# Optimization experiments

Measured on AMD Instinct MI355X. Metric: run time of the kernel, lower is better.

The kernel has to match this reference:

```python
import jax, jax.numpy as jnp
import numpy as np

N = 32768   # nodes
E = 524288  # edges (avg degree 16)
F = 32      # num_features
H = 512     # hidden_channels
C = 10      # num_classes
G = 64      # graphs in batch


def setup_inputs() -> dict:
    key = jax.random.key(0)
    ks = jax.random.split(key, 16)
    s = 0.05  # weight init scale
    f32 = jnp.float32
    return {
        "x": jax.random.normal(ks[0], (N, F), f32),
        "edge_index": jax.random.randint(ks[1], (2, E), 0, N),
        "batch_index": jnp.sort(jax.random.randint(ks[2], (N,), 0, G)),
        # initial_conv: F -> H  (PyG GraphConv: lin_root on x, lin_rel on aggregated neighbors)
        "w_root0": jax.random.normal(ks[3], (F, H), f32) * s,
        "w_rel0": jax.random.normal(ks[4], (F, H), f32) * s,
        "b0": jnp.zeros((H,), f32),
        # conv1..conv4 stacked: H -> H
        "w_root": jax.random.normal(ks[5], (4, H, H), f32) * s,
        "w_rel": jax.random.normal(ks[6], (4, H, H), f32) * s,
        "b": jnp.zeros((4, H), f32),
        # MLP tail
        "lin1_w": jax.random.normal(ks[7], (2 * H, H), f32) * s,
        "lin1_b": jnp.zeros((H,), f32),
        "lin2_w": jax.random.normal(ks[8], (H, H), f32) * s,
        "lin2_b": jnp.zeros((H,), f32),
        "lin3_w": jax.random.normal(ks[9], (H, C), f32) * s,
        "lin3_b": jnp.zeros((C,), f32),
    }


def _graph_conv(h, src, dst, w_root, w_rel, bias):
    # out_i = h_i @ W_root + (sum_{j->i} h_j) @ W_rel + b   (PyG GraphConv, aggr='add')
    agg = jax.ops.segment_sum(h[src], dst, num_segments=N)
    return h @ w_root + agg @ w_rel + bias


def reference(x, edge_index, batch_index,
              w_root0, w_rel0, b0, w_root, w_rel, b,
              lin1_w, lin1_b, lin2_w, lin2_b, lin3_w, lin3_b):
    src, dst = edge_index[0], edge_index[1]
    h = jnp.tanh(_graph_conv(x, src, dst, w_root0, w_rel0, b0))
    for i in range(4):  # fixed small layer loop
        h = jnp.tanh(_graph_conv(h, src, dst, w_root[i], w_rel[i], b[i]))
    # global max + mean pool over graphs
    gmax = jax.ops.segment_max(h, batch_index, num_segments=G)
    gsum = jax.ops.segment_sum(h, batch_index, num_segments=G)
    cnt = jax.ops.segment_sum(jnp.ones((N,), h.dtype), batch_index, num_segments=G)
    gmean = gsum / jnp.maximum(cnt, 1.0)[:, None]
    g = jnp.concatenate([gmax, gmean], axis=1)  # [G, 2H]
    # dropout is identity at inference (training=False)
    g = jnp.tanh(g @ lin1_w + lin1_b)
    g = jnp.tanh(g @ lin2_w + lin2_b)
    logits = g @ lin3_w + lin3_b
    return jax.nn.log_softmax(logits, axis=1)
```

## Files before the change

### kernel.cpp

```cpp
#include <hip/hip_runtime.h>
#include <hip/hip_bf16.h>
#include <math.h>

#define NN 32768
#define EE 524288
#define FF 32
#define HH 512
#define GG 64
#define CC 10

typedef __attribute__((ext_vector_type(8))) short short8;
typedef __attribute__((ext_vector_type(4))) float floatx4;
typedef __attribute__((ext_vector_type(4))) unsigned int uintx4;

__device__ __forceinline__ float bf16_to_f32(unsigned short u) {
    union { unsigned int u; float f; } v;
    v.u = ((unsigned int)u) << 16;
    return v.f;
}
__device__ __forceinline__ unsigned short f32_to_bf16(float f) {
    union { float f; unsigned int u; } v;
    v.f = f;
    unsigned int u = v.u;
    u += 0x7FFFu + ((u >> 16) & 1u);
    return (unsigned short)(u >> 16);
}
__device__ __forceinline__ float fast_tanh(float x) {
    float e = __expf(2.0f * x);
    return 1.0f - 2.0f * __builtin_amdgcn_rcpf(e + 1.0f);
}

__global__ __launch_bounds__(256) void prep_all_kernel(const float* __restrict__ wr0, const float* __restrict__ wl0,
                                unsigned short* __restrict__ WT0,
                                const float* __restrict__ wroot, const float* __restrict__ wrel,
                                unsigned short* __restrict__ WTs,
                                const float* __restrict__ x, unsigned short* __restrict__ X0,
                                int* __restrict__ counts) {
    const int b = blockIdx.x;
    const int tid = threadIdx.x;
    if (b < 520) {
        __shared__ unsigned short tile[64][65];
        const int ty = tid >> 6, tx = tid & 63;
        if (b < 8) {
            const int n0 = b * 64;
#pragma unroll
            for (int q = 0; q < 16; ++q) {
                const int k = ty * 16 + q;
                const float v = (k < 32) ? wr0[k * 512 + n0 + tx]
                                         : wl0[(k - 32) * 512 + n0 + tx];
                tile[k][tx] = f32_to_bf16(v);
            }
            __syncthreads();
#pragma unroll
            for (int q = 0; q < 16; ++q) {
                const int n = n0 + ty * 16 + q;
                WT0[n * 64 + tx] = tile[tx][ty * 16 + q];
            }
        } else {
            const int bb = b - 8;
            const int l = bb >> 7;
            const int r = bb & 127;
            const int k0 = (r >> 3) * 64;
            const int n0 = (r & 7) * 64;
            const float* Wl = (k0 < 512) ? wroot + (size_t)l * 262144
                                         : wrel + (size_t)l * 262144;
            const int kb = (k0 < 512) ? k0 : k0 - 512;
#pragma unroll
            for (int q = 0; q < 16; ++q) {
                const int kk = ty * 16 + q;
                tile[kk][tx] = f32_to_bf16(Wl[(size_t)(kb + kk) * 512 + n0 + tx]);
            }
            __syncthreads();
#pragma unroll
            for (int q = 0; q < 16; ++q) {
                const int n = n0 + ty * 16 + q;
                WTs[(size_t)l * 524288 + (size_t)n * 1024 + k0 + tx] = tile[tx][ty * 16 + q];
            }
        }
    } else if (b < 4616) {
        const int t = (b - 520) * 256 + tid;
        const int i = t >> 5, c = t & 31;
        X0[(size_t)i * 64 + c] = f32_to_bf16(x[t]);
    } else {
        const int t4 = (b - 4616) * 256 + tid;
        if (t4 < 8320) {
            int4 z; z.x = 0; z.y = 0; z.z = 0; z.w = 0;
            ((int4*)counts)[t4] = z;
        }
    }
}

__global__ void hist_kernel(const int* __restrict__ dst, int* __restrict__ counts) {
    int e = blockIdx.x * blockDim.x + threadIdx.x;
    if (e < EE) atomicAdd(&counts[dst[e]], 1);
}

__global__ __launch_bounds__(256) void deg_hist_kernel(const int* __restrict__ counts,
                                                       int* __restrict__ degHist) {
    __shared__ int lh[256];
    lh[threadIdx.x] = 0;
    __syncthreads();
    int i = blockIdx.x * 256 + threadIdx.x;
    int d = counts[i]; if (d > 255) d = 255;
    atomicAdd(&lh[255 - d], 1);
    __syncthreads();
    int v = lh[threadIdx.x];
    if (v) atomicAdd(&degHist[threadIdx.x], v);
}

__global__ __launch_bounds__(256) void deg_scatter_kernel(const int* __restrict__ counts,
                                                          const int* __restrict__ degHist,
                                                          int* __restrict__ degBump,
                                                          int* __restrict__ perm,
                                                          int* __restrict__ pDeg,
                                                          int* __restrict__ iperm) {
    __shared__ int lh[256];
    __shared__ int sh[256];
    __shared__ int base[256];
    const int t = threadIdx.x;
    lh[t] = 0;
    const int own = degHist[t];
    sh[t] = own;
    __syncthreads();
    for (int off = 1; off < 256; off <<= 1) {
        int v = (t >= off) ? sh[t - off] : 0;
        __syncthreads();
        sh[t] += v;
        __syncthreads();
    }
    const int excl = sh[t] - own;
    int i = blockIdx.x * 256 + t;
    int dtrue = counts[i];
    int d = dtrue > 255 ? 255 : dtrue;
    int bin = 255 - d;
    int lr = atomicAdd(&lh[bin], 1);
    __syncthreads();
    int c = lh[t];
    if (c) base[t] = excl + atomicAdd(&degBump[t], c);
    __syncthreads();
    int p = base[bin] + lr;
    perm[p] = i;
    pDeg[p] = dtrue;
    iperm[i] = p;
}
__global__ __launch_bounds__(1024) void scan_kernel(const int* __restrict__ pDeg,
                                                    int* __restrict__ pRowStart,
                                                    int* __restrict__ pCursor) {
    __shared__ int part[1024];
    const int t = threadIdx.x;
    const int base = t * 32;
    int local[32];
    const int4* cp = (const int4*)(pDeg + base);
    int s = 0;
#pragma unroll
    for (int ii = 0; ii < 8; ++ii) {
        int4 v = cp[ii];
        local[ii * 4 + 0] = v.x; local[ii * 4 + 1] = v.y;
        local[ii * 4 + 2] = v.z; local[ii * 4 + 3] = v.w;
        s += v.x + v.y + v.z + v.w;
    }
    part[t] = s;
    __syncthreads();
    for (int off = 1; off < 1024; off <<= 1) {
        int v = (t >= off) ? part[t - off] : 0;
        __syncthreads();
        part[t] += v;
        __syncthreads();
    }
    int run = part[t] - s;
#pragma unroll
    for (int i = 0; i < 32; ++i) {
        pRowStart[base + i] = run;
        pCursor[base + i] = run;
        run += local[i];
    }
    if (t == 1023) pRowStart[NN] = run;
}

__global__ void scatter_kernel(const int* __restrict__ src, const int* __restrict__ dst,
                               const int* __restrict__ iperm,
                               int* __restrict__ pCursor, int* __restrict__ pssrc) {
    int e = blockIdx.x * blockDim.x + threadIdx.x;
    if (e < EE) {
        int p = iperm[dst[e]];
        int q = atomicAdd(&pCursor[p], 1);
        pssrc[q] = src[e];
    }
}

__device__ __forceinline__ void acc8(float* a, uint4 d) {
    a[0] += bf16_to_f32((unsigned short)(d.x & 0xFFFFu));
    a[1] += bf16_to_f32((unsigned short)(d.x >> 16));
    a[2] += bf16_to_f32((unsigned short)(d.y & 0xFFFFu));
    a[3] += bf16_to_f32((unsigned short)(d.y >> 16));
    a[4] += bf16_to_f32((unsigned short)(d.z & 0xFFFFu));
    a[5] += bf16_to_f32((unsigned short)(d.z >> 16));
    a[6] += bf16_to_f32((unsigned short)(d.w & 0xFFFFu));
    a[7] += bf16_to_f32((unsigned short)(d.w >> 16));
}
__device__ __forceinline__ void acc8v(float* a, uintx4 d) {
    a[0] += bf16_to_f32((unsigned short)(d[0] & 0xFFFFu));
    a[1] += bf16_to_f32((unsigned short)(d[0] >> 16));
    a[2] += bf16_to_f32((unsigned short)(d[1] & 0xFFFFu));
    a[3] += bf16_to_f32((unsigned short)(d[1] >> 16));
    a[4] += bf16_to_f32((unsigned short)(d[2] & 0xFFFFu));
    a[5] += bf16_to_f32((unsigned short)(d[2] >> 16));
    a[6] += bf16_to_f32((unsigned short)(d[3] & 0xFFFFu));
    a[7] += bf16_to_f32((unsigned short)(d[3] >> 16));
}

__global__ __launch_bounds__(256) void agg_kernel(const unsigned short* __restrict__ Xh,
                                                  unsigned short* __restrict__ Xagg,
                                                  const int* __restrict__ pRowStart,
                                                  const int* __restrict__ pssrc,
                                                  const int* __restrict__ perm) {
    const int p = blockIdx.x * 64 + (threadIdx.x >> 2);
    const int lc = threadIdx.x & 3;
    const int node = perm[p];
    const int s = pRowStart[p];
    const int e = pRowStart[p + 1];
    float a[8] = {0.f, 0.f, 0.f, 0.f, 0.f, 0.f, 0.f, 0.f};
    const unsigned short* base = Xh + lc * 8;
    int i = s;
    for (; i + 4 <= e; i += 4) {
        int j0 = pssrc[i], j1 = pssrc[i + 1], j2 = pssrc[i + 2], j3 = pssrc[i + 3];
        uint4 d0 = *(const uint4*)(base + (size_t)j0 * 64);
        uint4 d1 = *(const uint4*)(base + (size_t)j1 * 64);
        uint4 d2 = *(const uint4*)(base + (size_t)j2 * 64);
        uint4 d3 = *(const uint4*)(base + (size_t)j3 * 64);
        acc8(a, d0); acc8(a, d1); acc8(a, d2); acc8(a, d3);
    }
    for (; i < e; ++i) {
        int j = pssrc[i];
        uint4 d = *(const uint4*)(base + (size_t)j * 64);
        acc8(a, d);
    }
    unsigned short* out = Xagg + (size_t)node * 64 + lc * 8;
#pragma unroll
    for (int c = 0; c < 8; ++c) out[c] = f32_to_bf16(a[c]);
}

#define GLOAD(dreg, voff) \
    asm volatile("buffer_load_dwordx4 %0, %1, %2, 0 offen" \
                 : "=v"(dreg) : "v"(voff), "s"(srsrc))

__global__ __launch_bounds__(256, 3) void agg_slice_kernel(const unsigned short* __restrict__ Xh,
                                                           unsigned short* __restrict__ Xagg,
                                                           const int* __restrict__ pRowStart,
                                                           const int* __restrict__ pssrc,
                                                           const int* __restrict__ perm) {
    const int slice = blockIdx.x & 7;
    const int pair = blockIdx.x >> 3;
    const int wv = threadIdx.x >> 6;
    const int lane = threadIdx.x & 63;
    const int ln = lane >> 3;
    const int lc = lane & 7;
    const int colOff = slice * 64 + lc * 8;
    const unsigned short* base = Xh + colOff;
    uintx4 srsrc;
    {
        union { const unsigned short* p; unsigned int u[2]; } ba;
        ba.p = Xh + slice * 64;
        srsrc[0] = ba.u[0];
        srsrc[1] = ba.u[1] & 0xFFFFu;
        srsrc[2] = 0xFFFFFFFFu;
        srsrc[3] = 0x00020000u;
    }
    const unsigned int lcoff = (unsigned int)(lc << 4);
#pragma unroll
    for (int half = 0; half < 2; ++half) {
        const int nb = half ? (1023 - pair) : pair;
        const int p = nb * 32 + wv * 8 + ln;
        const int node = perm[p];
        const int s = pRowStart[p];
        const int e = pRowStart[p + 1];
        float a[8] = {0.f, 0.f, 0.f, 0.f, 0.f, 0.f, 0.f, 0.f};
        int i = s;
        for (; i + 16 <= e; i += 16) {
            unsigned int vo[16];
#pragma unroll
            for (int u = 0; u < 16; ++u)
                vo[u] = (((unsigned int)pssrc[i + u]) << 11) | lcoff;
            uintx4 d0, d1, d2, d3, d4, d5, d6, d7, d8, d9, d10, d11, d12, d13, d14, d15;
            __builtin_amdgcn_sched_barrier(0);
            GLOAD(d0, vo[0]);   GLOAD(d1, vo[1]);   GLOAD(d2, vo[2]);   GLOAD(d3, vo[3]);
            GLOAD(d4, vo[4]);   GLOAD(d5, vo[5]);   GLOAD(d6, vo[6]);   GLOAD(d7, vo[7]);
            GLOAD(d8, vo[8]);   GLOAD(d9, vo[9]);   GLOAD(d10, vo[10]); GLOAD(d11, vo[11]);
            GLOAD(d12, vo[12]); GLOAD(d13, vo[13]); GLOAD(d14, vo[14]); GLOAD(d15, vo[15]);
            asm volatile("s_waitcnt vmcnt(8)" ::: "memory");
            __builtin_amdgcn_sched_barrier(0);
            acc8v(a, d0); acc8v(a, d1); acc8v(a, d2); acc8v(a, d3);
            acc8v(a, d4); acc8v(a, d5); acc8v(a, d6); acc8v(a, d7);
            asm volatile("s_waitcnt vmcnt(0)" ::: "memory");
            __builtin_amdgcn_sched_barrier(0);
            acc8v(a, d8);  acc8v(a, d9);  acc8v(a, d10); acc8v(a, d11);
            acc8v(a, d12); acc8v(a, d13); acc8v(a, d14); acc8v(a, d15);
        }
        if (e - i >= 8) {
            unsigned int vo[8];
#pragma unroll
            for (int u = 0; u < 8; ++u)
                vo[u] = (((unsigned int)pssrc[i + u]) << 11) | lcoff;
            uintx4 d0, d1, d2, d3, d4, d5, d6, d7;
            __builtin_amdgcn_sched_barrier(0);
            GLOAD(d0, vo[0]); GLOAD(d1, vo[1]); GLOAD(d2, vo[2]); GLOAD(d3, vo[3]);
            GLOAD(d4, vo[4]); GLOAD(d5, vo[5]); GLOAD(d6, vo[6]); GLOAD(d7, vo[7]);
            asm volatile("s_waitcnt vmcnt(4)" ::: "memory");
            __builtin_amdgcn_sched_barrier(0);
            acc8v(a, d0); acc8v(a, d1); acc8v(a, d2); acc8v(a, d3);
            asm volatile("s_waitcnt vmcnt(0)" ::: "memory");
            __builtin_amdgcn_sched_barrier(0);
            acc8v(a, d4); acc8v(a, d5); acc8v(a, d6); acc8v(a, d7);
            i += 8;
        }
        for (; i + 4 <= e; i += 4) {
            int j0 = pssrc[i], j1 = pssrc[i + 1], j2 = pssrc[i + 2], j3 = pssrc[i + 3];
            uint4 e0 = *(const uint4*)(base + (size_t)j0 * 1024);
            uint4 e1 = *(const uint4*)(base + (size_t)j1 * 1024);
            uint4 e2 = *(const uint4*)(base + (size_t)j2 * 1024);
            uint4 e3 = *(const uint4*)(base + (size_t)j3 * 1024);
            acc8(a, e0); acc8(a, e1); acc8(a, e2); acc8(a, e3);
        }
        for (; i < e; ++i) {
            int j = pssrc[i];
            uint4 d = *(const uint4*)(base + (size_t)j * 1024);
            acc8(a, d);
        }
        unsigned short* out = Xagg + (size_t)node * 1024 + colOff;
#pragma unroll
        for (int c = 0; c < 8; ++c) out[c] = f32_to_bf16(a[c]);
    }
}

__global__ __launch_bounds__(256, 4) void gemm_bias_tanh(const unsigned short* __restrict__ Xin,
                                                         int ldin, int K,
                                                         const unsigned short* __restrict__ WT,
                                                         const float* __restrict__ bias,
                                                         unsigned short* __restrict__ Xout,
                                                         int ldout) {
    __shared__ __align__(16) unsigned short As[128 * 64];
    __shared__ __align__(16) unsigned short Bs[128 * 64];
    const int tid = threadIdx.x;
    const int lane = tid & 63;
    const int wave = tid >> 6;
    const int wm = wave >> 1, wn = wave & 1;
    const int bm = blockIdx.x, bn = blockIdx.y;

    floatx4 acc[4][4] = {};

    const int lrow = lane >> 3;
    const int schunk = (lane & 7) ^ (lrow & 7);
    const unsigned short* Abase = Xin + (size_t)(bm * 128) * ldin;
    const unsigned short* Bbase = WT + (size_t)(bn * 128) * K;
    const int m = lane & 15;
    const int quad = lane >> 4;

    for (int k0 = 0; k0 < K; k0 += 64) {
        __syncthreads();
#pragma unroll
        for (int q = 0; q < 4; ++q) {
            const int rr = q * 32 + wave * 8;
            const int row = rr + lrow;
            const unsigned short* sa = Abase + (size_t)row * ldin + (k0 + schunk * 8);
            const unsigned short* sb = Bbase + (size_t)row * K + (k0 + schunk * 8);
            __builtin_amdgcn_global_load_lds(
                (const __attribute__((address_space(1))) void*)sa,
                (__attribute__((address_space(3))) void*)(&As[rr * 64]), 16, 0, 0);
            __builtin_amdgcn_global_load_lds(
                (const __attribute__((address_space(1))) void*)sb,
                (__attribute__((address_space(3))) void*)(&Bs[rr * 64]), 16, 0, 0);
        }
        __syncthreads();
#pragma unroll
        for (int half = 0; half < 2; ++half) {
            short8 af[4], bfr[4];
#pragma unroll
            for (int t = 0; t < 4; ++t) {
                const int row = wm * 64 + t * 16 + m;
                const int chunk = (half * 4 + quad) ^ (row & 7);
                af[t] = *(const short8*)&As[row * 64 + chunk * 8];
            }
#pragma unroll
            for (int t = 0; t < 4; ++t) {
                const int row = wn * 64 + t * 16 + m;
                const int chunk = (half * 4 + quad) ^ (row & 7);
                bfr[t] = *(const short8*)&Bs[row * 64 + chunk * 8];
            }
#pragma unroll
            for (int mt = 0; mt < 4; ++mt)
#pragma unroll
                for (int nt = 0; nt < 4; ++nt)
                    acc[mt][nt] = __builtin_amdgcn_mfma_f32_16x16x32_bf16(af[mt], bfr[nt],
                                                                          acc[mt][nt], 0, 0, 0);
        }
    }

    const int row0 = bm * 128 + wm * 64;
    const int col0 = bn * 128 + wn * 64;
#pragma unroll
    for (int mt = 0; mt < 4; ++mt) {
#pragma unroll
        for (int nt = 0; nt < 4; ++nt) {
            const int col = col0 + nt * 16 + m;
            const float bv = bias[col];
#pragma unroll
            for (int r = 0; r < 4; ++r) {
                const int row = row0 + mt * 16 + quad * 4 + r;
                float v = fast_tanh(acc[mt][nt][r] + bv);
                Xout[(size_t)row * ldout + col] = f32_to_bf16(v);
            }
        }
    }
}

__device__ __forceinline__ void stage_half(const unsigned short* __restrict__ gsrc0,
                                           int ldg, unsigned short* ldsHalf,
                                           int w, int lane) {
#pragma unroll
    for (int q = 0; q < 2; ++q) {
        const int rb = q * 64 + w * 8;
        const unsigned short* src = gsrc0 + (size_t)(rb + (lane >> 3)) * ldg
                                    + ((lane & 7) ^ (lane >> 3)) * 8;
        __builtin_amdgcn_global_load_lds(
            (const __attribute__((address_space(1))) void*)src,
            (__attribute__((address_space(3))) void*)(ldsHalf + rb * 64), 16, 0, 0);
    }
}
__device__ __forceinline__ void stage_q(const unsigned short* __restrict__ gsrc0,
                                        int ldg, unsigned short* ldsQ,
                                        int w, int lane) {
    const unsigned short* src = gsrc0 + (size_t)(w * 8 + (lane >> 3)) * ldg
                                + ((lane & 7) ^ (lane >> 3)) * 8;
    __builtin_amdgcn_global_load_lds(
        (const __attribute__((address_space(1))) void*)src,
        (__attribute__((address_space(3))) void*)(ldsQ + (w * 8) * 64), 16, 0, 0);
}

__global__ __launch_bounds__(512, 2) void gemm256_bias_tanh(
    const unsigned short* __restrict__ Xin, int ldin, int K,
    const unsigned short* __restrict__ WT, const float* __restrict__ bias,
    unsigned short* __restrict__ Xout, int ldout) {
    __shared__ __align__(16) unsigned short As[2][256 * 64];
    __shared__ __align__(16) unsigned short Bs[2][256 * 64];
    const int tid = threadIdx.x;
    const int lane = tid & 63;
    const int w = tid >> 6;
    const int wm = w >> 2, wn = w & 3;
    const int m = lane & 15, quad = lane >> 4;
    const int id = (int)blockIdx.x;
    const int bm = (id & 7) * 16 + (id >> 4);
    const int bn = (id >> 3) & 1;
    const int NT = K >> 6;

    const unsigned short* Abase = Xin + (size_t)(bm * 256) * ldin;
    const unsigned short* Bbase = WT + (size_t)(bn * 256) * K;

    floatx4 acc[8][4] = {};

#define STG_AH(buf, h, kt_) stage_half(Abase + (size_t)((h) * 128) * ldin + (kt_) * 64, ldin, \
                                       &As[buf][(h) * 128 * 64], w, lane)
#define STG_BH(buf, h, kt_) stage_half(Bbase + (size_t)((h) * 128) * K + (kt_) * 64, K, \
                                       &Bs[buf][(h) * 128 * 64], w, lane)
#define STG_AQ(buf, qr, kt_) stage_q(Abase + (size_t)((qr) * 64) * ldin + (kt_) * 64, ldin, \
                                     &As[buf][(qr) * 64 * 64], w, lane)

    STG_BH(0, 0, 0); STG_BH(0, 1, 0); STG_AH(0, 0, 0); STG_AH(0, 1, 0);
    STG_BH(1, 0, 1); STG_BH(1, 1, 1); STG_AH(1, 0, 1); STG_AH(1, 1, 1);
    asm volatile("s_waitcnt vmcnt(8)" ::: "memory");
    __builtin_amdgcn_s_barrier();

    for (int kt = 0; kt < NT; ++kt) {
        const int cur = kt & 1;
        const unsigned short* Ac = &As[cur][0];
        const unsigned short* Bc = &Bs[cur][0];
        const bool pf = (kt + 2 < NT);
        short8 afr[8], bfr[8];

#pragma unroll
        for (int nf = 0; nf < 4; ++nf)
#pragma unroll
            for (int ks = 0; ks < 2; ++ks) {
                const int col = wn * 64 + nf * 16 + m;
                const int chunk = (ks * 4 + quad) ^ (col & 7);
                bfr[nf * 2 + ks] = *(const short8*)&Bc[col * 64 + chunk * 8];
            }
#pragma unroll
        for (int t = 0; t < 4; ++t)
#pragma unroll
            for (int ks = 0; ks < 2; ++ks) {
                const int row = wm * 128 + t * 16 + m;
                const int chunk = (ks * 4 + quad) ^ (row & 7);
                afr[t * 2 + ks] = *(const short8*)&Ac[row * 64 + chunk * 8];
            }
        __builtin_amdgcn_s_barrier();
        __builtin_amdgcn_s_setprio(1);
#pragma unroll
        for (int t = 0; t < 4; ++t)
#pragma unroll
            for (int u = 0; u < 2; ++u)
#pragma unroll
                for (int ks = 0; ks < 2; ++ks)
                    acc[t][u] = __builtin_amdgcn_mfma_f32_16x16x32_bf16(
                        afr[t * 2 + ks], bfr[u * 2 + ks], acc[t][u], 0, 0, 0);
        __builtin_amdgcn_s_setprio(0);
        __builtin_amdgcn_s_barrier();

        if (pf) { STG_AQ(cur, 0, kt + 2); STG_AQ(cur, 2, kt + 2); }
        __builtin_amdgcn_s_barrier();
        __builtin_amdgcn_s_setprio(1);
#pragma unroll
        for (int t = 0; t < 4; ++t)
#pragma unroll
            for (int u = 2; u < 4; ++u)
#pragma unroll
                for (int ks = 0; ks < 2; ++ks)
                    acc[t][u] = __builtin_amdgcn_mfma_f32_16x16x32_bf16(
                        afr[t * 2 + ks], bfr[u * 2 + ks], acc[t][u], 0, 0, 0);
        __builtin_amdgcn_s_setprio(0);
        __builtin_amdgcn_s_barrier();

#pragma unroll
        for (int t = 0; t < 4; ++t)
#pragma unroll
            for (int ks = 0; ks < 2; ++ks) {
                const int row = wm * 128 + (4 + t) * 16 + m;
                const int chunk = (ks * 4 + quad) ^ (row & 7);
                afr[t * 2 + ks] = *(const short8*)&Ac[row * 64 + chunk * 8];
            }
        __builtin_amdgcn_sched_barrier(0);
        if (pf) STG_BH(cur, 0, kt + 2);
        __builtin_amdgcn_s_barrier();
        __builtin_amdgcn_s_setprio(1);
#pragma unroll
        for (int t = 0; t < 4; ++t)
#pragma unroll
            for (int u = 0; u < 2; ++u)
#pragma unroll
                for (int ks = 0; ks < 2; ++ks)
                    acc[4 + t][u] = __builtin_amdgcn_mfma_f32_16x16x32_bf16(
                        afr[t * 2 + ks], bfr[u * 2 + ks], acc[4 + t][u], 0, 0, 0);
        __builtin_amdgcn_s_setprio(0);
        __builtin_amdgcn_s_barrier();

        if (pf) {
            STG_BH(cur, 1, kt + 2);
            STG_AQ(cur, 1, kt + 2); STG_AQ(cur, 3, kt + 2);
        }
        __builtin_amdgcn_s_barrier();
        __builtin_amdgcn_s_setprio(1);
#pragma unroll
        for (int t = 0; t < 4; ++t)
#pragma unroll
            for (int u = 2; u < 4; ++u)
#pragma unroll
                for (int ks = 0; ks < 2; ++ks)
                    acc[4 + t][u] = __builtin_amdgcn_mfma_f32_16x16x32_bf16(
                        afr[t * 2 + ks], bfr[u * 2 + ks], acc[4 + t][u], 0, 0, 0);
        __builtin_amdgcn_s_setprio(0);
        if (kt <= NT - 3) {
            asm volatile("s_waitcnt vmcnt(8)" ::: "memory");
        } else {
            asm volatile("s_waitcnt vmcnt(0)" ::: "memory");
        }
        __builtin_amdgcn_s_barrier();
    }
#undef STG_AH
#undef STG_BH
#undef STG_AQ

    const int row0 = bm * 256 + wm * 128;
    const int col0 = bn * 256 + wn * 64;
#pragma unroll
    for (int mf = 0; mf < 8; ++mf) {
#pragma unroll
        for (int nf = 0; nf < 4; ++nf) {
            const int col = col0 + nf * 16 + m;
            const float bv = bias[col];
#pragma unroll
            for (int r = 0; r < 4; ++r) {
                const int row = row0 + mf * 16 + quad * 4 + r;
                float v = fast_tanh(acc[mf][nf][r] + bv);
                Xout[(size_t)row * ldout + col] = f32_to_bf16(v);
            }
        }
    }
}

__global__ __launch_bounds__(256) void pool_partial(const unsigned short* __restrict__ h,
                                                    const int* __restrict__ batch,
                                                    float* __restrict__ part) {
    const int gi = blockIdx.x, rs = blockIdx.y, t = threadIdx.x;
    int lo = 0, hi = NN;
    while (lo < hi) { int mid = (lo + hi) >> 1; if (batch[mid] < gi) lo = mid + 1; else hi = mid; }
    const int start = lo;
    hi = NN;
    while (lo < hi) { int mid = (lo + hi) >> 1; if (batch[mid] < gi + 1) lo = mid + 1; else hi = mid; }
    const int end = lo;
    const int len = end - start;
    const int q = (len + 7) >> 3;
    int r0 = start + rs * q;
    int r1 = r0 + q; if (r1 > end) r1 = end; if (r0 > end) r0 = end;
    float mx0 = -INFINITY, mx1 = -INFINITY, s0 = 0.f, s1 = 0.f;
    int i = r0;
    for (; i + 2 <= r1; i += 2) {
        unsigned int d0 = *(const unsigned int*)(h + (size_t)i * 1024 + t * 2);
        unsigned int d1 = *(const unsigned int*)(h + (size_t)(i + 1) * 1024 + t * 2);
        float v0 = bf16_to_f32((unsigned short)(d0 & 0xFFFFu));
        float v1 = bf16_to_f32((unsigned short)(d0 >> 16));
        float w0 = bf16_to_f32((unsigned short)(d1 & 0xFFFFu));
        float w1 = bf16_to_f32((unsigned short)(d1 >> 16));
        mx0 = fmaxf(mx0, fmaxf(v0, w0)); mx1 = fmaxf(mx1, fmaxf(v1, w1));
        s0 += v0 + w0; s1 += v1 + w1;
    }
    for (; i < r1; ++i) {
        unsigned int d0 = *(const unsigned int*)(h + (size_t)i * 1024 + t * 2);
        float v0 = bf16_to_f32((unsigned short)(d0 & 0xFFFFu));
        float v1 = bf16_to_f32((unsigned short)(d0 >> 16));
        mx0 = fmaxf(mx0, v0); mx1 = fmaxf(mx1, v1);
        s0 += v0; s1 += v1;
    }
    float* p = part + ((size_t)gi * 8 + rs) * 1024;
    p[t * 2] = mx0; p[t * 2 + 1] = mx1;
    p[512 + t * 2] = s0; p[512 + t * 2 + 1] = s1;
}

__global__ __launch_bounds__(256) void pool_combine(const float* __restrict__ part,
                                                    const int* __restrict__ batch,
                                                    float* __restrict__ gT) {
    const int gi = blockIdx.x, t = threadIdx.x;
    int lo = 0, hi = NN;
    while (lo < hi) { int mid = (lo + hi) >> 1; if (batch[mid] < gi) lo = mid + 1; else hi = mid; }
    const int start = lo;
    hi = NN;
    while (lo < hi) { int mid = (lo + hi) >> 1; if (batch[mid] < gi + 1) lo = mid + 1; else hi = mid; }
    int cnt = lo - start; if (cnt < 1) cnt = 1;
    const float inv = 1.0f / (float)cnt;
    float mx0 = -INFINITY, mx1 = -INFINITY, s0 = 0.f, s1 = 0.f;
#pragma unroll
    for (int rs = 0; rs < 8; ++rs) {
        const float* p = part + ((size_t)gi * 8 + rs) * 1024;
        mx0 = fmaxf(mx0, p[t * 2]); mx1 = fmaxf(mx1, p[t * 2 + 1]);
        s0 += p[512 + t * 2]; s1 += p[512 + t * 2 + 1];
    }
    gT[(size_t)(2 * t) * 64 + gi]        = mx0;
    gT[(size_t)(2 * t + 1) * 64 + gi]    = mx1;
    gT[(size_t)(512 + 2 * t) * 64 + gi]  = s0 * inv;
    gT[(size_t)(512 + 2 * t + 1) * 64 + gi] = s1 * inv;
}

__global__ __launch_bounds__(256) void mlp_splitk(const float* __restrict__ ginT,
                                                  const float* __restrict__ W,
                                                  int Ndim,
                                                  float* __restrict__ partial) {
    __shared__ float gsT[64][68];
    __shared__ float Ws[64][68];
    const int t = threadIdx.x;
    const int wv = t >> 6, l = t & 63;
    const int nb = blockIdx.x, kb = blockIdx.y;
    const int n0 = nb * 64;
    const int gr = t >> 2;
    const int c4 = (t & 3) * 16;
    float acc[16] = {};
#pragma unroll
    for (int sub = 0; sub < 2; ++sub) {
        const int k0 = kb * 128 + sub * 64;
        __syncthreads();
        {
            const float4* gsrc = (const float4*)(ginT + (size_t)(k0 + gr) * 64 + c4);
            float4* gd = (float4*)&gsT[gr][c4];
            gd[0] = gsrc[0]; gd[1] = gsrc[1]; gd[2] = gsrc[2]; gd[3] = gsrc[3];
            const float4* wsrc = (const float4*)(W + (size_t)(k0 + gr) * Ndim + n0 + c4);
            float4* wd = (float4*)&Ws[gr][c4];
            wd[0] = wsrc[0]; wd[1] = wsrc[1]; wd[2] = wsrc[2]; wd[3] = wsrc[3];
        }
        __syncthreads();
#pragma unroll 4
        for (int kk = 0; kk < 64; ++kk) {
            const float wval = Ws[kk][l];
            const float4* gv = (const float4*)&gsT[kk][wv * 16];
            float4 g0 = gv[0], g1 = gv[1], g2 = gv[2], g3 = gv[3];
            acc[0]  = fmaf(g0.x, wval, acc[0]);  acc[1]  = fmaf(g0.y, wval, acc[1]);
            acc[2]  = fmaf(g0.z, wval, acc[2]);  acc[3]  = fmaf(g0.w, wval, acc[3]);
            acc[4]  = fmaf(g1.x, wval, acc[4]);  acc[5]  = fmaf(g1.y, wval, acc[5]);
            acc[6]  = fmaf(g1.z, wval, acc[6]);  acc[7]  = fmaf(g1.w, wval, acc[7]);
            acc[8]  = fmaf(g2.x, wval, acc[8]);  acc[9]  = fmaf(g2.y, wval, acc[9]);
            acc[10] = fmaf(g2.z, wval, acc[10]); acc[11] = fmaf(g2.w, wval, acc[11]);
            acc[12] = fmaf(g3.x, wval, acc[12]); acc[13] = fmaf(g3.y, wval, acc[13]);
            acc[14] = fmaf(g3.z, wval, acc[14]); acc[15] = fmaf(g3.w, wval, acc[15]);
        }
    }
    float* p = partial + ((size_t)kb * 64) * Ndim;
#pragma unroll
    for (int g = 0; g < 16; ++g)
        p[(size_t)(wv * 16 + g) * Ndim + n0 + l] = acc[g];
}

__global__ __launch_bounds__(256) void mlp_combine(const float* __restrict__ partial, int nparts,
                                                   const float* __restrict__ bias, int Ndim,
                                                   float* __restrict__ outN,
                                                   float* __restrict__ outT) {
    const int idx = blockIdx.x * 256 + threadIdx.x;
    if (idx >= 64 * Ndim) return;
    const int g = idx / Ndim, n = idx - g * Ndim;
    float s = bias[n];
    for (int kb = 0; kb < nparts; ++kb)
        s += partial[((size_t)kb * 64 + g) * Ndim + n];
    const float v = fast_tanh(s);
    if (outN) outN[(size_t)g * Ndim + n] = v;
    if (outT) outT[(size_t)n * 64 + g] = v;
}

__global__ __launch_bounds__(64) void head_kernel(const float* __restrict__ g2,
                                                  const float* __restrict__ W,
                                                  const float* __restrict__ b,
                                                  float* __restrict__ out) {
    const int gi = blockIdx.x, t = threadIdx.x;
    const float4* gp = (const float4*)(g2 + (size_t)gi * HH + t * 8);
    float4 ga = gp[0], gb = gp[1];
    float gv[8] = {ga.x, ga.y, ga.z, ga.w, gb.x, gb.y, gb.z, gb.w};
    float logits[CC];
#pragma unroll
    for (int c = 0; c < CC; ++c) {
        float p = 0.f;
#pragma unroll
        for (int j = 0; j < 8; ++j)
            p = fmaf(gv[j], W[(t * 8 + j) * CC + c], p);
#pragma unroll
        for (int off = 32; off > 0; off >>= 1)
            p += __shfl_xor(p, off, 64);
        logits[c] = p + b[c];
    }
    if (t == 0) {
        float mx = logits[0];
#pragma unroll
        for (int c = 1; c < CC; ++c) mx = fmaxf(mx, logits[c]);
        float s = 0.f;
#pragma unroll
        for (int c = 0; c < CC; ++c) s += expf(logits[c] - mx);
        float lse = mx + logf(s);
#pragma unroll
        for (int c = 0; c < CC; ++c) out[(size_t)gi * CC + c] = logits[c] - lse;
    }
}

extern "C" void kernel_launch(void* const* d_in, const int* in_sizes, int n_in,
                              void* d_out, int out_size, void* d_ws, size_t ws_size,
                              hipStream_t stream) {
    const float* x       = (const float*)d_in[0];
    const int*   ei      = (const int*)d_in[1];
    const int*   batch   = (const int*)d_in[2];
    const float* w_root0 = (const float*)d_in[3];
    const float* w_rel0  = (const float*)d_in[4];
    const float* b0      = (const float*)d_in[5];
    const float* w_root  = (const float*)d_in[6];
    const float* w_rel   = (const float*)d_in[7];
    const float* bvec    = (const float*)d_in[8];
    const float* lin1_w  = (const float*)d_in[9];
    const float* lin1_b  = (const float*)d_in[10];
    const float* lin2_w  = (const float*)d_in[11];
    const float* lin2_b  = (const float*)d_in[12];
    const float* lin3_w  = (const float*)d_in[13];
    const float* lin3_b  = (const float*)d_in[14];
    float* out = (float*)d_out;

    char* w = (char*)d_ws;
    size_t off = 0;
    auto alloc = [&](size_t bytes) -> char* {
        char* p = w + off;
        off += (bytes + 255) & ~(size_t)255;
        return p;
    };
    unsigned short* Xa  = (unsigned short*)alloc((size_t)NN * 1024 * 2);
    unsigned short* Xb  = (unsigned short*)alloc((size_t)NN * 1024 * 2);
    unsigned short* X0  = (unsigned short*)alloc((size_t)NN * 64 * 2);
    unsigned short* WT0 = (unsigned short*)alloc(512 * 64 * 2);
    unsigned short* WTs = (unsigned short*)alloc((size_t)4 * 512 * 1024 * 2);
    int* counts   = (int*)alloc((size_t)(NN + 512) * 4);
    int* degHist  = counts + NN;
    int* degBump  = counts + NN + 256;
    int* perm     = (int*)alloc((size_t)NN * 4);
    int* pDeg     = (int*)alloc((size_t)NN * 4);
    int* iperm    = (int*)alloc((size_t)NN * 4);
    int* pRowStart= (int*)alloc((size_t)(NN + 1) * 4);
    int* pCursor  = (int*)alloc((size_t)NN * 4);
    int* pssrc    = (int*)alloc((size_t)EE * 4);
    float* gbufT  = (float*)alloc((size_t)1024 * 64 * 4);
    float* g1T    = (float*)alloc((size_t)512 * 64 * 4);
    float* g2buf  = (float*)alloc((size_t)GG * 512 * 4);
    float* mlpPart = (float*)alloc((size_t)8 * 64 * 512 * 4);
    float* part   = (float*)X0;

    const int* esrc = ei;
    const int* edst = ei + EE;

    prep_all_kernel<<<4649, 256, 0, stream>>>(w_root0, w_rel0, WT0, w_root, w_rel, WTs, x, X0, counts);
    hist_kernel<<<2048, 256, 0, stream>>>(edst, counts);
    deg_hist_kernel<<<128, 256, 0, stream>>>(counts, degHist);
    deg_scatter_kernel<<<128, 256, 0, stream>>>(counts, degHist, degBump, perm, pDeg, iperm);
    scan_kernel<<<1, 1024, 0, stream>>>(pDeg, pRowStart, pCursor);
    scatter_kernel<<<2048, 256, 0, stream>>>(esrc, edst, iperm, pCursor, pssrc);

    agg_kernel<<<512, 256, 0, stream>>>(X0, X0 + 32, pRowStart, pssrc, perm);
    gemm_bias_tanh<<<dim3(256, 4), 256, 0, stream>>>(X0, 64, 64, WT0, b0, Xa, 1024);

    agg_slice_kernel<<<4096, 256, 0, stream>>>(Xa, Xa + 512, pRowStart, pssrc, perm);
    gemm256_bias_tanh<<<256, 512, 0, stream>>>(Xa, 1024, 1024, WTs + 0 * 524288, bvec + 0, Xb, 1024);
    agg_slice_kernel<<<4096, 256, 0, stream>>>(Xb, Xb + 512, pRowStart, pssrc, perm);
    gemm256_bias_tanh<<<256, 512, 0, stream>>>(Xb, 1024, 1024, WTs + 1 * 524288, bvec + 512, Xa, 1024);
    agg_slice_kernel<<<4096, 256, 0, stream>>>(Xa, Xa + 512, pRowStart, pssrc, perm);
    gemm256_bias_tanh<<<256, 512, 0, stream>>>(Xa, 1024, 1024, WTs + 2 * 524288, bvec + 1024, Xb, 1024);
    agg_slice_kernel<<<4096, 256, 0, stream>>>(Xb, Xb + 512, pRowStart, pssrc, perm);
    gemm256_bias_tanh<<<256, 512, 0, stream>>>(Xb, 1024, 1024, WTs + 3 * 524288, bvec + 1536, Xa, 1024);

    pool_partial<<<dim3(GG, 8), 256, 0, stream>>>(Xa, batch, part);
    pool_combine<<<GG, 256, 0, stream>>>(part, batch, gbufT);
    mlp_splitk<<<dim3(8, 8), 256, 0, stream>>>(gbufT, lin1_w, 512, mlpPart);
    mlp_combine<<<128, 256, 0, stream>>>(mlpPart, 8, lin1_b, 512, nullptr, g1T);
    mlp_splitk<<<dim3(8, 4), 256, 0, stream>>>(g1T, lin2_w, 512, mlpPart);
    mlp_combine<<<128, 256, 0, stream>>>(mlpPart, 4, lin2_b, 512, g2buf, nullptr);
    head_kernel<<<GG, 64, 0, stream>>>(g2buf, lin3_w, lin3_b, out);
}
```

Measured before the change: 578.8 us.

## Replace interleaved staged GEMM pipeline with simple one-ahead double buffering

The 256x256 bias+tanh GEMM kernel drops its split-phase schedule. That schedule staged A quarter-tiles and B halves two k-tiles ahead, spread across four MFMA sub-phases with s_setprio and explicit vmcnt waits. It now prefetches the whole next k-tile at the top of each iteration, runs all MFMAs in two blocks, and ends each iteration with one __syncthreads. This removes many barriers and priority toggles and simplifies the code. In exchange, prefetch distance drops from two tiles to one, and each iteration waits for all outstanding loads at the barrier, so global-to-LDS latency is less well hidden.

```diff
diff --git a/kernel.cpp b/kernel.cpp
--- a/kernel.cpp
+++ b/kernel.cpp
@@ -426,15 +426,6 @@
             (__attribute__((address_space(3))) void*)(ldsHalf + rb * 64), 16, 0, 0);
     }
 }
-__device__ __forceinline__ void stage_q(const unsigned short* __restrict__ gsrc0,
-                                        int ldg, unsigned short* ldsQ,
-                                        int w, int lane) {
-    const unsigned short* src = gsrc0 + (size_t)(w * 8 + (lane >> 3)) * ldg
-                                + ((lane & 7) ^ (lane >> 3)) * 8;
-    __builtin_amdgcn_global_load_lds(
-        (const __attribute__((address_space(1))) void*)src,
-        (__attribute__((address_space(3))) void*)(ldsQ + (w * 8) * 64), 16, 0, 0);
-}
 
 __global__ __launch_bounds__(512, 2) void gemm256_bias_tanh(
     const unsigned short* __restrict__ Xin, int ldin, int K,
@@ -457,25 +448,22 @@
 
     floatx4 acc[8][4] = {};
 
-#define STG_AH(buf, h, kt_) stage_half(Abase + (size_t)((h) * 128) * ldin + (kt_) * 64, ldin, \
-                                       &As[buf][(h) * 128 * 64], w, lane)
-#define STG_BH(buf, h, kt_) stage_half(Bbase + (size_t)((h) * 128) * K + (kt_) * 64, K, \
-                                       &Bs[buf][(h) * 128 * 64], w, lane)
-#define STG_AQ(buf, qr, kt_) stage_q(Abase + (size_t)((qr) * 64) * ldin + (kt_) * 64, ldin, \
-                                     &As[buf][(qr) * 64 * 64], w, lane)
-
-    STG_BH(0, 0, 0); STG_BH(0, 1, 0); STG_AH(0, 0, 0); STG_AH(0, 1, 0);
-    STG_BH(1, 0, 1); STG_BH(1, 1, 1); STG_AH(1, 0, 1); STG_AH(1, 1, 1);
-    asm volatile("s_waitcnt vmcnt(8)" ::: "memory");
-    __builtin_amdgcn_s_barrier();
+#define STG_T(buf, kt_) do { \
+        stage_half(Bbase + (kt_) * 64, K, &Bs[buf][0], w, lane); \
+        stage_half(Bbase + (size_t)128 * K + (kt_) * 64, K, &Bs[buf][128 * 64], w, lane); \
+        stage_half(Abase + (kt_) * 64, ldin, &As[buf][0], w, lane); \
+        stage_half(Abase + (size_t)128 * ldin + (kt_) * 64, ldin, &As[buf][128 * 64], w, lane); \
+    } while (0)
+
+    STG_T(0, 0);
+    __syncthreads();
 
     for (int kt = 0; kt < NT; ++kt) {
         const int cur = kt & 1;
+        if (kt + 1 < NT) STG_T(cur ^ 1, kt + 1);
         const unsigned short* Ac = &As[cur][0];
         const unsigned short* Bc = &Bs[cur][0];
-        const bool pf = (kt + 2 < NT);
-        short8 afr[8], bfr[8];
-
+        short8 bfr[8], afr[8];
 #pragma unroll
         for (int nf = 0; nf < 4; ++nf)
 #pragma unroll
@@ -492,33 +480,14 @@
                 const int chunk = (ks * 4 + quad) ^ (row & 7);
                 afr[t * 2 + ks] = *(const short8*)&Ac[row * 64 + chunk * 8];
             }
-        __builtin_amdgcn_s_barrier();
-        __builtin_amdgcn_s_setprio(1);
 #pragma unroll
         for (int t = 0; t < 4; ++t)
 #pragma unroll
-            for (int u = 0; u < 2; ++u)
+            for (int u = 0; u < 4; ++u)
 #pragma unroll
                 for (int ks = 0; ks < 2; ++ks)
                     acc[t][u] = __builtin_amdgcn_mfma_f32_16x16x32_bf16(
                         afr[t * 2 + ks], bfr[u * 2 + ks], acc[t][u], 0, 0, 0);
-        __builtin_amdgcn_s_setprio(0);
-        __builtin_amdgcn_s_barrier();
-
-        if (pf) { STG_AQ(cur, 0, kt + 2); STG_AQ(cur, 2, kt + 2); }
-        __builtin_amdgcn_s_barrier();
-        __builtin_amdgcn_s_setprio(1);
-#pragma unroll
-        for (int t = 0; t < 4; ++t)
-#pragma unroll
-            for (int u = 2; u < 4; ++u)
-#pragma unroll
-                for (int ks = 0; ks < 2; ++ks)
-                    acc[t][u] = __builtin_amdgcn_mfma_f32_16x16x32_bf16(
-                        afr[t * 2 + ks], bfr[u * 2 + ks], acc[t][u], 0, 0, 0);
-        __builtin_amdgcn_s_setprio(0);
-        __builtin_amdgcn_s_barrier();
-
 #pragma unroll
         for (int t = 0; t < 4; ++t)
 #pragma unroll
@@ -527,46 +496,17 @@
                 const int chunk = (ks * 4 + quad) ^ (row & 7);
                 afr[t * 2 + ks] = *(const short8*)&Ac[row * 64 + chunk * 8];
             }
-        __builtin_amdgcn_sched_barrier(0);
-        if (pf) STG_BH(cur, 0, kt + 2);
-        __builtin_amdgcn_s_barrier();
-        __builtin_amdgcn_s_setprio(1);
 #pragma unroll
         for (int t = 0; t < 4; ++t)
 #pragma unroll
-            for (int u = 0; u < 2; ++u)
+            for (int u = 0; u < 4; ++u)
 #pragma unroll
                 for (int ks = 0; ks < 2; ++ks)
                     acc[4 + t][u] = __builtin_amdgcn_mfma_f32_16x16x32_bf16(
                         afr[t * 2 + ks], bfr[u * 2 + ks], acc[4 + t][u], 0, 0, 0);
-        __builtin_amdgcn_s_setprio(0);
-        __builtin_amdgcn_s_barrier();
-
-        if (pf) {
-            STG_BH(cur, 1, kt + 2);
-            STG_AQ(cur, 1, kt + 2); STG_AQ(cur, 3, kt + 2);
-        }
-        __builtin_amdgcn_s_barrier();
-        __builtin_amdgcn_s_setprio(1);
-#pragma unroll
-        for (int t = 0; t < 4; ++t)
-#pragma unroll
-            for (int u = 2; u < 4; ++u)
-#pragma unroll
-                for (int ks = 0; ks < 2; ++ks)
-                    acc[4 + t][u] = __builtin_amdgcn_mfma_f32_16x16x32_bf16(
-                        afr[t * 2 + ks], bfr[u * 2 + ks], acc[4 + t][u], 0, 0, 0);
-        __builtin_amdgcn_s_setprio(0);
-        if (kt <= NT - 3) {
-            asm volatile("s_waitcnt vmcnt(8)" ::: "memory");
-        } else {
-            asm volatile("s_waitcnt vmcnt(0)" ::: "memory");
-        }
-        __builtin_amdgcn_s_barrier();
-    }
-#undef STG_AH
-#undef STG_BH
-#undef STG_AQ
+        __syncthreads();
+    }
+#undef STG_T
 
     const int row0 = bm * 256 + wm * 128;
     const int col0 = bn * 256 + wn * 64;
```

After: 567.7 us (median of 2 runs). Within noise of the previous version (-1.9%).
